# Optimization experiments

Hardware: AMD Instinct MI355X
Metric: run time of the kernel (lower is better)

The kernel has to match this reference:

```python
import jax, jax.numpy as jnp
import numpy as np

RRELU_SLOPE = (1.0 / 8.0 + 1.0 / 3.0) / 2.0  # RReLU eval-mode negative slope


def _layer(h, edge_feats, src, dst, W, b, Lw, Lb, n_nodes):
    # per-edge message: concat(src node feat, edge feat) -> linear
    msg = jnp.concatenate([h[src], edge_feats], axis=-1) @ W + b  # [E, H]
    # mean-aggregate messages by destination node (0 for isolated nodes, DGL semantics)
    s = jax.ops.segment_sum(msg, dst, num_segments=n_nodes)  # [N, H]
    cnt = jax.ops.segment_sum(jnp.ones((dst.shape[0], 1), msg.dtype), dst,
                              num_segments=n_nodes)  # [N, 1]
    agg = jnp.where(cnt > 0, s / jnp.maximum(cnt, 1.0), 0.0)
    # self-loop linear add
    agg = agg + h @ Lw + Lb
    # RReLU (eval mode = leaky relu with slope (lower+upper)/2); dropout p=0 is identity
    return jnp.where(agg >= 0, agg, agg * RRELU_SLOPE)


def setup_inputs() -> dict:
    key = jax.random.key(0)
    ks = jax.random.split(key, 12)
    N, E, D, H = 50000, 640000, 128, 128
    sc_in = 1.0 / np.sqrt(2 * D)
    sc_d = 1.0 / np.sqrt(D)
    sc_o = 1.0 / np.sqrt(2 * H)
    return {
        "node_feats": jax.random.normal(ks[0], (N, D), jnp.float32),
        "edge_feats": jax.random.normal(ks[1], (E, D), jnp.float32),
        "src": jax.random.randint(ks[2], (E,), 0, N),
        "dst": jax.random.randint(ks[3], (E,), 0, N),
        "W1": jax.random.uniform(ks[4], (2 * D, H), jnp.float32, -sc_in, sc_in),
        "b1": jnp.zeros((H,), jnp.float32),
        "L1": jax.random.uniform(ks[5], (D, H), jnp.float32, -sc_d, sc_d),
        "lb1": jnp.zeros((H,), jnp.float32),
        "W2": jax.random.uniform(ks[6], (2 * H, H), jnp.float32, -sc_in, sc_in),
        "b2": jnp.zeros((H,), jnp.float32),
        "L2": jax.random.uniform(ks[7], (H, H), jnp.float32, -sc_d, sc_d),
        "lb2": jnp.zeros((H,), jnp.float32),
        "Wo": jax.random.uniform(ks[8], (2 * H, H), jnp.float32, -sc_o, sc_o),
        "bo": jnp.zeros((H,), jnp.float32),
    }


def reference(node_feats, edge_feats, src, dst, W1, b1, L1, lb1, W2, b2, L2, lb2, Wo, bo):
    n = node_feats.shape[0]
    h1 = _layer(node_feats, edge_feats, src, dst, W1, b1, L1, lb1, n)
    h2 = _layer(h1, edge_feats, src, dst, W2, b2, L2, lb2, n)
    multihop = jnp.concatenate([h1, h2], axis=-1)  # [N, 2H]
    return multihop @ Wo + bo
```

## Files before the change

### kernel.cpp

```cpp
#include <hip/hip_runtime.h>
#include <hip/hip_bf16.h>

typedef unsigned short u16;
typedef unsigned int   u32;

using bf16x8 = __attribute__((ext_vector_type(8))) __bf16;
using f32x4  = __attribute__((ext_vector_type(4))) float;

#define SLOPE 0.22916666666666666f
#define CAP 64

static __device__ __forceinline__ u16 f2bf(float f) {
    u32 u = __float_as_uint(f);
    u += 0x7fffu + ((u >> 16) & 1u);
    return (u16)(u >> 16);
}
static __device__ __forceinline__ float bf2f(u16 h) {
    return __uint_as_float(((u32)h) << 16);
}

static __device__ __forceinline__ void gload_lds16(const u16* g, u16* l) {
    __builtin_amdgcn_global_load_lds(
        (const __attribute__((address_space(1))) void*)g,
        (__attribute__((address_space(3))) void*)l,
        16, 0, 0);
}

static __device__ __forceinline__ void add8(float* a, uint4 u) {
    a[0] += bf2f((u16)u.x); a[1] += bf2f((u16)(u.x >> 16));
    a[2] += bf2f((u16)u.y); a[3] += bf2f((u16)(u.y >> 16));
    a[4] += bf2f((u16)u.z); a[5] += bf2f((u16)(u.z >> 16));
    a[6] += bf2f((u16)u.w); a[7] += bf2f((u16)(u.w >> 16));
}

__global__ void k_prep(const int* __restrict__ src, const int* __restrict__ dst,
                       int* __restrict__ deg, int2* __restrict__ se,
                       const float* __restrict__ node, u16* __restrict__ nfb,
                       const float* __restrict__ W1, const float* __restrict__ L1,
                       const float* __restrict__ W2, const float* __restrict__ L2,
                       const float* __restrict__ Wo, u16* __restrict__ T,
                       int E, int n8, int gE, int gF) {
    int b = blockIdx.x, t = threadIdx.x;
    if (b < gE) {
        int i = b * 256 + t;
        if (i < E) {
            int d = dst[i];
            int p = atomicAdd(&deg[d], 1);
            if (p < CAP) se[(size_t)d * CAP + p] = make_int2(src[i], i);
        }
    } else if (b < gE + gF) {
        int i = (b - gE) * 256 + t;
        if (i < n8) {
            const float4* p = (const float4*)node + (size_t)i * 2;
            float4 a = p[0], c = p[1];
            union { u16 u[8]; uint4 v; } pk;
            pk.u[0] = f2bf(a.x); pk.u[1] = f2bf(a.y); pk.u[2] = f2bf(a.z); pk.u[3] = f2bf(a.w);
            pk.u[4] = f2bf(c.x); pk.u[5] = f2bf(c.y); pk.u[6] = f2bf(c.z); pk.u[7] = f2bf(c.w);
            *((uint4*)nfb + i) = pk.v;
        }
    } else {
        int m = b - gE - gF;
        const float* S; int rowoff;
        switch (m) {
            case 0: S = W1; rowoff = 0;   break;
            case 1: S = W1; rowoff = 128; break;
            case 2: S = L1; rowoff = 0;   break;
            case 3: S = W2; rowoff = 0;   break;
            case 4: S = W2; rowoff = 128; break;
            case 5: S = L2; rowoff = 0;   break;
            case 6: S = Wo; rowoff = 0;   break;
            default: S = Wo; rowoff = 128; break;
        }
        u16* O = T + m * 16384;
        for (int i = t; i < 16384; i += 256) {
            int c = i >> 7, k = i & 127;
            O[i] = f2bf(S[(rowoff + k) * 128 + c]);
        }
    }
}

__global__ void k_aggf(const float* __restrict__ ef, const u16* __restrict__ nfb,
                       const int2* __restrict__ se, const int* __restrict__ deg,
                       u16* __restrict__ EF, u16* __restrict__ A, int N) {
    int w = (blockIdx.x * blockDim.x + threadIdx.x) >> 6;
    int lane = threadIdx.x & 63;
    if (w >= N) return;
    int t4 = lane >> 4, qq = lane & 15;
    int d = deg[w];
    int dc = d < CAP ? d : CAP;
    const int2* sp = se + (size_t)w * CAP;
    float e[8] = {0.f, 0.f, 0.f, 0.f, 0.f, 0.f, 0.f, 0.f};
    float n[8] = {0.f, 0.f, 0.f, 0.f, 0.f, 0.f, 0.f, 0.f};
    int i = 0;
    for (; i + 8 <= dc; i += 8) {
        int2 iA = sp[i + t4], iB = sp[i + 4 + t4];
        const float* ra = ef + (size_t)iA.y * 128 + qq * 8;
        const float* rb = ef + (size_t)iB.y * 128 + qq * 8;
        float4 a0 = *(const float4*)ra, a1 = *(const float4*)(ra + 4);
        float4 c0 = *(const float4*)rb, c1 = *(const float4*)(rb + 4);
        uint4 ua = *(const uint4*)(nfb + (size_t)iA.x * 128 + qq * 8);
        uint4 ub = *(const uint4*)(nfb + (size_t)iB.x * 128 + qq * 8);
        e[0] += a0.x + c0.x; e[1] += a0.y + c0.y; e[2] += a0.z + c0.z; e[3] += a0.w + c0.w;
        e[4] += a1.x + c1.x; e[5] += a1.y + c1.y; e[6] += a1.z + c1.z; e[7] += a1.w + c1.w;
        add8(n, ua); add8(n, ub);
    }
    for (; i + 4 <= dc; i += 4) {
        int2 iA = sp[i + t4];
        const float* ra = ef + (size_t)iA.y * 128 + qq * 8;
        float4 a0 = *(const float4*)ra, a1 = *(const float4*)(ra + 4);
        uint4 ua = *(const uint4*)(nfb + (size_t)iA.x * 128 + qq * 8);
        e[0] += a0.x; e[1] += a0.y; e[2] += a0.z; e[3] += a0.w;
        e[4] += a1.x; e[5] += a1.y; e[6] += a1.z; e[7] += a1.w;
        add8(n, ua);
    }
    if (i + t4 < dc) {
        int2 iA = sp[i + t4];
        const float* ra = ef + (size_t)iA.y * 128 + qq * 8;
        float4 a0 = *(const float4*)ra, a1 = *(const float4*)(ra + 4);
        uint4 ua = *(const uint4*)(nfb + (size_t)iA.x * 128 + qq * 8);
        e[0] += a0.x; e[1] += a0.y; e[2] += a0.z; e[3] += a0.w;
        e[4] += a1.x; e[5] += a1.y; e[6] += a1.z; e[7] += a1.w;
        add8(n, ua);
    }
    #pragma unroll
    for (int j = 0; j < 8; j++) {
        e[j] += __shfl_xor(e[j], 16); e[j] += __shfl_xor(e[j], 32);
        n[j] += __shfl_xor(n[j], 16); n[j] += __shfl_xor(n[j], 32);
    }
    float sc = d > 0 ? 1.0f / (float)d : 0.0f;
    if (t4 == 0) {
        union { u16 u[8]; uint4 v; } pk;
        #pragma unroll
        for (int j = 0; j < 8; j++) pk.u[j] = f2bf(e[j] * sc);
        *(uint4*)(EF + (size_t)w * 128 + qq * 8) = pk.v;
    } else if (t4 == 1) {
        union { u16 u[8]; uint4 v; } pk;
        #pragma unroll
        for (int j = 0; j < 8; j++) pk.u[j] = f2bf(n[j] * sc);
        *(uint4*)(A + (size_t)w * 128 + qq * 8) = pk.v;
    }
}

__global__ void k_aggb(const u16* __restrict__ h, const int2* __restrict__ se,
                       const int* __restrict__ deg, u16* __restrict__ out, int N) {
    int w = (blockIdx.x * blockDim.x + threadIdx.x) >> 6;
    int lane = threadIdx.x & 63;
    if (w >= N) return;
    int quarter = lane >> 4, q = lane & 15;
    int d = deg[w];
    int dc = d < CAP ? d : CAP;
    const int2* sp = se + (size_t)w * CAP;
    float a[8] = {0.f, 0.f, 0.f, 0.f, 0.f, 0.f, 0.f, 0.f};
    int i = 0;
    for (; i + 8 <= dc; i += 8) {
        int eA = sp[i + quarter].x, eB = sp[i + 4 + quarter].x;
        uint4 uA = *(const uint4*)(h + (size_t)eA * 128 + q * 8);
        uint4 uB = *(const uint4*)(h + (size_t)eB * 128 + q * 8);
        add8(a, uA); add8(a, uB);
    }
    for (; i + 4 <= dc; i += 4) {
        int eA = sp[i + quarter].x;
        uint4 uA = *(const uint4*)(h + (size_t)eA * 128 + q * 8);
        add8(a, uA);
    }
    if (i + quarter < dc) {
        int eA = sp[i + quarter].x;
        uint4 uA = *(const uint4*)(h + (size_t)eA * 128 + q * 8);
        add8(a, uA);
    }
    #pragma unroll
    for (int j = 0; j < 8; j++) {
        a[j] += __shfl_xor(a[j], 32);
        a[j] += __shfl_xor(a[j], 16);
    }
    if (quarter == 0) {
        float sc = d > 0 ? 1.0f / (float)d : 0.0f;
        union { u16 u[8]; uint4 v; } pk;
        #pragma unroll
        for (int j = 0; j < 8; j++) pk.u[j] = f2bf(a[j] * sc);
        *(uint4*)(out + (size_t)w * 128 + q * 8) = pk.v;
    }
}

#define STAGE_X128(LBUF, GPTR)                                                      \
    {                                                                               \
        _Pragma("unroll")                                                           \
        for (int i_ = 0; i_ < 4; i_++) {                                            \
            int id_ = t + i_ * 512;                                                 \
            int r_ = id_ >> 4, c16_ = id_ & 15;                                     \
            int rg_ = row0 + r_; if (rg_ >= N) rg_ = N - 1;                         \
            gload_lds16((GPTR) + (size_t)rg_ * 128 + ((c16_ ^ (r_ & 15)) << 3),     \
                        (LBUF) + id_ * 8);                                          \
        }                                                                           \
    }
#define STAGE_W512(GPTR)                                                            \
    {                                                                               \
        _Pragma("unroll")                                                           \
        for (int i_ = 0; i_ < 4; i_++) {                                            \
            int id_ = t + i_ * 512;                                                 \
            int cc_ = id_ >> 4, c16_ = id_ & 15;                                    \
            gload_lds16((GPTR) + cc_ * 128 + ((c16_ ^ (cc_ & 15)) << 3),            \
                        Wl + id_ * 8);                                              \
        }                                                                           \
    }
#define COMPUTE(LBUF)                                                               \
    {                                                                               \
        _Pragma("unroll")                                                           \
        for (int ks_ = 0; ks_ < 4; ks_++) {                                         \
            bf16x8 af_[2], bf_[4];                                                  \
            _Pragma("unroll")                                                       \
            for (int h_ = 0; h_ < 2; h_++) {                                        \
                int r_ = wr * 32 + h_ * 16 + lanelo;                                \
                int ch_ = (ks_ * 4 + lanehi) ^ (r_ & 15);                           \
                af_[h_] = *(const bf16x8*)((LBUF) + r_ * 128 + ch_ * 8);            \
            }                                                                       \
            _Pragma("unroll")                                                       \
            for (int g_ = 0; g_ < 4; g_++) {                                        \
                int cc_ = wc * 64 + g_ * 16 + lanelo;                               \
                int ch_ = (ks_ * 4 + lanehi) ^ (cc_ & 15);                          \
                bf_[g_] = *(const bf16x8*)(Wl + cc_ * 128 + ch_ * 8);               \
            }                                                                       \
            _Pragma("unroll")                                                       \
            for (int h_ = 0; h_ < 2; h_++)                                          \
                _Pragma("unroll")                                                   \
                for (int g_ = 0; g_ < 4; g_++)                                      \
                    acc[h_][g_] = __builtin_amdgcn_mfma_f32_16x16x32_bf16(          \
                        af_[h_], bf_[g_], acc[h_][g_], 0, 0, 0);                    \
        }                                                                           \
    }

__global__ __launch_bounds__(512, 4) void k_gemm3s(
    const u16* __restrict__ X0, const u16* __restrict__ X1, const u16* __restrict__ X2,
    const u16* __restrict__ T0, const u16* __restrict__ T1, const u16* __restrict__ T2,
    const float* __restrict__ bm, const int* __restrict__ deg,
    const float* __restrict__ ba, u16* __restrict__ outp, int N) {

    __shared__ u16 XB[128 * 128];
    __shared__ u16 Wl[128 * 128];

    int t = threadIdx.x, lane = t & 63, wid = t >> 6;
    int lanelo = lane & 15, lanehi = lane >> 4;
    int wr = wid >> 1, wc = wid & 1;
    int row0 = blockIdx.x * 128;

    f32x4 acc[2][4];
    #pragma unroll
    for (int h = 0; h < 2; h++)
        #pragma unroll
        for (int g = 0; g < 4; g++) acc[h][g] = (f32x4){0.f, 0.f, 0.f, 0.f};

    STAGE_X128(XB, X0);
    STAGE_W512(T0);
    __syncthreads();
    COMPUTE(XB);
    __syncthreads();
    STAGE_X128(XB, X1);
    STAGE_W512(T1);
    __syncthreads();
    COMPUTE(XB);
    __syncthreads();
    STAGE_X128(XB, X2);
    STAGE_W512(T2);
    __syncthreads();
    COMPUTE(XB);

    #pragma unroll
    for (int h = 0; h < 2; h++) {
        #pragma unroll
        for (int r = 0; r < 4; r++) {
            int rowt = wr * 32 + h * 16 + lanehi * 4 + r;
            int rg = row0 + rowt;
            if (rg >= N) continue;
            float m = (deg[rg] > 0) ? 1.f : 0.f;
            #pragma unroll
            for (int g = 0; g < 4; g++) {
                int col = wc * 64 + g * 16 + lanelo;
                float v = acc[h][g][r] + ba[col] + m * bm[col];
                v = (v >= 0.f) ? v : v * SLOPE;
                outp[(size_t)rg * 128 + col] = f2bf(v);
            }
        }
    }
}

__global__ __launch_bounds__(512, 4) void k_gemmo(
    const u16* __restrict__ X0, const u16* __restrict__ X1,
    const u16* __restrict__ T0, const u16* __restrict__ T1,
    const float* __restrict__ ba, float* __restrict__ outp, int N) {

    __shared__ u16 XB[128 * 128];
    __shared__ u16 Wl[128 * 128];

    int t = threadIdx.x, lane = t & 63, wid = t >> 6;
    int lanelo = lane & 15, lanehi = lane >> 4;
    int wr = wid >> 1, wc = wid & 1;
    int row0 = blockIdx.x * 128;

    f32x4 acc[2][4];
    #pragma unroll
    for (int h = 0; h < 2; h++)
        #pragma unroll
        for (int g = 0; g < 4; g++) acc[h][g] = (f32x4){0.f, 0.f, 0.f, 0.f};

    STAGE_X128(XB, X0);
    STAGE_W512(T0);
    __syncthreads();
    COMPUTE(XB);
    __syncthreads();
    STAGE_X128(XB, X1);
    STAGE_W512(T1);
    __syncthreads();
    COMPUTE(XB);

    #pragma unroll
    for (int h = 0; h < 2; h++) {
        #pragma unroll
        for (int r = 0; r < 4; r++) {
            int rowt = wr * 32 + h * 16 + lanehi * 4 + r;
            int rg = row0 + rowt;
            if (rg >= N) continue;
            #pragma unroll
            for (int g = 0; g < 4; g++) {
                int col = wc * 64 + g * 16 + lanelo;
                outp[(size_t)rg * 128 + col] = acc[h][g][r] + ba[col];
            }
        }
    }
}


extern "C" void kernel_launch(void* const* d_in, const int* in_sizes, int n_in,
                              void* d_out, int out_size, void* d_ws, size_t ws_size,
                              hipStream_t stream) {
    const float* node = (const float*)d_in[0];
    const float* ef   = (const float*)d_in[1];
    const int*   src  = (const int*)d_in[2];
    const int*   dst  = (const int*)d_in[3];
    const float* W1   = (const float*)d_in[4];
    const float* b1   = (const float*)d_in[5];
    const float* L1   = (const float*)d_in[6];
    const float* lb1  = (const float*)d_in[7];
    const float* W2   = (const float*)d_in[8];
    const float* b2   = (const float*)d_in[9];
    const float* L2   = (const float*)d_in[10];
    const float* lb2  = (const float*)d_in[11];
    const float* Wo   = (const float*)d_in[12];
    const float* bo   = (const float*)d_in[13];
    int N = in_sizes[0] / 128;
    int E = in_sizes[2];

    char* ws = (char*)d_ws;
    size_t o = 0;
    auto alloc = [&](size_t bytes) {
        void* p = ws + o;
        o = (o + bytes + 511) & ~(size_t)511;
        return p;
    };
    int*  deg = (int*)alloc((size_t)N * 4);
    int2* se  = (int2*)alloc((size_t)N * CAP * 8);
    u16*  T   = (u16*)alloc((size_t)8 * 16384 * 2);
    u16*  nfb = (u16*)alloc((size_t)N * 128 * 2);
    u16*  EF  = (u16*)alloc((size_t)N * 128 * 2);
    u16*  A   = (u16*)alloc((size_t)N * 128 * 2);
    u16*  h1  = (u16*)alloc((size_t)N * 128 * 2);
    u16*  h2  = (u16*)alloc((size_t)N * 128 * 2);

    hipMemsetAsync(deg, 0, (size_t)N * 4, stream);

    int gE = (E + 255) / 256;
    int n8 = N * 128 / 8;
    int gF = (n8 + 255) / 256;
    k_prep<<<gE + gF + 8, 256, 0, stream>>>(src, dst, deg, se, node, nfb,
                                            W1, L1, W2, L2, Wo, T, E, n8, gE, gF);

    int gA = (N + 3) / 4;
    k_aggf<<<gA, 256, 0, stream>>>(ef, nfb, se, deg, EF, A, N);

    int gb = (N + 127) / 128;
    k_gemm3s<<<gb, 512, 0, stream>>>(A, EF, nfb, T, T + 16384, T + 2 * 16384,
                                     b1, deg, lb1, h1, N);
    k_aggb<<<gA, 256, 0, stream>>>(h1, se, deg, A, N);
    k_gemm3s<<<gb, 512, 0, stream>>>(A, EF, h1, T + 3 * 16384, T + 4 * 16384, T + 5 * 16384,
                                     b2, deg, lb2, h2, N);
    k_gemmo<<<gb, 512, 0, stream>>>(h1, h2, T + 6 * 16384, T + 7 * 16384,
                                    bo, (float*)d_out, N);
}
```

Measured before the change: 203.4 us.

## Store only edge ids in CSR buckets and look up src indirectly

The per-destination bucket array now holds only the edge index instead of an (src, edge) pair, which halves its size and the scatter writes in the prep kernel. The aggregation kernels fetch the source node through an extra dependent load from the src array. The prep fill has each thread handle two edges to overlap atomics, and the weight transpose is split across 64 blocks instead of 8. The trade-off is an extra indirect gather latency in both aggregation kernels, set against less write traffic during prep.

```diff
diff --git a/kernel.cpp b/kernel.cpp
--- a/kernel.cpp
+++ b/kernel.cpp
@@ -33,23 +33,26 @@
     a[6] += bf2f((u16)u.w); a[7] += bf2f((u16)(u.w >> 16));
 }
 
-__global__ void k_prep(const int* __restrict__ src, const int* __restrict__ dst,
-                       int* __restrict__ deg, int2* __restrict__ se,
-                       const float* __restrict__ node, u16* __restrict__ nfb,
+__global__ void k_prep(const int* __restrict__ dst, int* __restrict__ deg,
+                       int* __restrict__ se, const float* __restrict__ node,
+                       u16* __restrict__ nfb,
                        const float* __restrict__ W1, const float* __restrict__ L1,
                        const float* __restrict__ W2, const float* __restrict__ L2,
                        const float* __restrict__ Wo, u16* __restrict__ T,
-                       int E, int n8, int gE, int gF) {
+                       int E, int halfE, int n8, int gFill, int gF) {
     int b = blockIdx.x, t = threadIdx.x;
-    if (b < gE) {
-        int i = b * 256 + t;
-        if (i < E) {
-            int d = dst[i];
-            int p = atomicAdd(&deg[d], 1);
-            if (p < CAP) se[(size_t)d * CAP + p] = make_int2(src[i], i);
-        }
-    } else if (b < gE + gF) {
-        int i = (b - gE) * 256 + t;
+    if (b < gFill) {
+        int i0 = b * 256 + t;
+        int i1 = i0 + halfE;
+        int d0 = -1, d1 = -1;
+        if (i0 < halfE) d0 = dst[i0];
+        if (i1 < E)     d1 = dst[i1];
+        int p0 = (d0 >= 0) ? atomicAdd(&deg[d0], 1) : 0;
+        int p1 = (d1 >= 0) ? atomicAdd(&deg[d1], 1) : 0;
+        if (d0 >= 0 && p0 < CAP) se[(size_t)d0 * CAP + p0] = i0;
+        if (d1 >= 0 && p1 < CAP) se[(size_t)d1 * CAP + p1] = i1;
+    } else if (b < gFill + gF) {
+        int i = (b - gFill) * 256 + t;
         if (i < n8) {
             const float4* p = (const float4*)node + (size_t)i * 2;
             float4 a = p[0], c = p[1];
@@ -59,7 +62,8 @@
             *((uint4*)nfb + i) = pk.v;
         }
     } else {
-        int m = b - gE - gF;
+        int mb = b - gFill - gF;
+        int m = mb >> 3, chunk = mb & 7;
         const float* S; int rowoff;
         switch (m) {
             case 0: S = W1; rowoff = 0;   break;
@@ -72,15 +76,17 @@
             default: S = Wo; rowoff = 128; break;
         }
         u16* O = T + m * 16384;
-        for (int i = t; i < 16384; i += 256) {
-            int c = i >> 7, k = i & 127;
-            O[i] = f2bf(S[(rowoff + k) * 128 + c]);
+        int j0 = chunk * 2048, j1 = j0 + 2048;
+        for (int j = j0 + t; j < j1; j += 256) {
+            int c = j >> 7, k = j & 127;
+            O[j] = f2bf(S[(rowoff + k) * 128 + c]);
         }
     }
 }
 
 __global__ void k_aggf(const float* __restrict__ ef, const u16* __restrict__ nfb,
-                       const int2* __restrict__ se, const int* __restrict__ deg,
+                       const int* __restrict__ se, const int* __restrict__ srcA,
+                       const int* __restrict__ deg,
                        u16* __restrict__ EF, u16* __restrict__ A, int N) {
     int w = (blockIdx.x * blockDim.x + threadIdx.x) >> 6;
     int lane = threadIdx.x & 63;
@@ -88,36 +94,39 @@
     int t4 = lane >> 4, qq = lane & 15;
     int d = deg[w];
     int dc = d < CAP ? d : CAP;
-    const int2* sp = se + (size_t)w * CAP;
+    const int* sp = se + (size_t)w * CAP;
     float e[8] = {0.f, 0.f, 0.f, 0.f, 0.f, 0.f, 0.f, 0.f};
     float n[8] = {0.f, 0.f, 0.f, 0.f, 0.f, 0.f, 0.f, 0.f};
     int i = 0;
     for (; i + 8 <= dc; i += 8) {
-        int2 iA = sp[i + t4], iB = sp[i + 4 + t4];
-        const float* ra = ef + (size_t)iA.y * 128 + qq * 8;
-        const float* rb = ef + (size_t)iB.y * 128 + qq * 8;
+        int eA = sp[i + t4], eB = sp[i + 4 + t4];
+        int sA = srcA[eA], sB = srcA[eB];
+        const float* ra = ef + (size_t)eA * 128 + qq * 8;
+        const float* rb = ef + (size_t)eB * 128 + qq * 8;
         float4 a0 = *(const float4*)ra, a1 = *(const float4*)(ra + 4);
         float4 c0 = *(const float4*)rb, c1 = *(const float4*)(rb + 4);
-        uint4 ua = *(const uint4*)(nfb + (size_t)iA.x * 128 + qq * 8);
-        uint4 ub = *(const uint4*)(nfb + (size_t)iB.x * 128 + qq * 8);
+        uint4 ua = *(const uint4*)(nfb + (size_t)sA * 128 + qq * 8);
+        uint4 ub = *(const uint4*)(nfb + (size_t)sB * 128 + qq * 8);
         e[0] += a0.x + c0.x; e[1] += a0.y + c0.y; e[2] += a0.z + c0.z; e[3] += a0.w + c0.w;
         e[4] += a1.x + c1.x; e[5] += a1.y + c1.y; e[6] += a1.z + c1.z; e[7] += a1.w + c1.w;
         add8(n, ua); add8(n, ub);
     }
     for (; i + 4 <= dc; i += 4) {
-        int2 iA = sp[i + t4];
-        const float* ra = ef + (size_t)iA.y * 128 + qq * 8;
+        int eA = sp[i + t4];
+        int sA = srcA[eA];
+        const float* ra = ef + (size_t)eA * 128 + qq * 8;
         float4 a0 = *(const float4*)ra, a1 = *(const float4*)(ra + 4);
-        uint4 ua = *(const uint4*)(nfb + (size_t)iA.x * 128 + qq * 8);
+        uint4 ua = *(const uint4*)(nfb + (size_t)sA * 128 + qq * 8);
         e[0] += a0.x; e[1] += a0.y; e[2] += a0.z; e[3] += a0.w;
         e[4] += a1.x; e[5] += a1.y; e[6] += a1.z; e[7] += a1.w;
         add8(n, ua);
     }
     if (i + t4 < dc) {
-        int2 iA = sp[i + t4];
-        const float* ra = ef + (size_t)iA.y * 128 + qq * 8;
+        int eA = sp[i + t4];
+        int sA = srcA[eA];
+        const float* ra = ef + (size_t)eA * 128 + qq * 8;
         float4 a0 = *(const float4*)ra, a1 = *(const float4*)(ra + 4);
-        uint4 ua = *(const uint4*)(nfb + (size_t)iA.x * 128 + qq * 8);
+        uint4 ua = *(const uint4*)(nfb + (size_t)sA * 128 + qq * 8);
         e[0] += a0.x; e[1] += a0.y; e[2] += a0.z; e[3] += a0.w;
         e[4] += a1.x; e[5] += a1.y; e[6] += a1.z; e[7] += a1.w;
         add8(n, ua);
@@ -141,31 +150,32 @@
     }
 }
 
-__global__ void k_aggb(const u16* __restrict__ h, const int2* __restrict__ se,
-                       const int* __restrict__ deg, u16* __restrict__ out, int N) {
+__global__ void k_aggb(const u16* __restrict__ h, const int* __restrict__ se,
+                       const int* __restrict__ srcA, const int* __restrict__ deg,
+                       u16* __restrict__ out, int N) {
     int w = (blockIdx.x * blockDim.x + threadIdx.x) >> 6;
     int lane = threadIdx.x & 63;
     if (w >= N) return;
     int quarter = lane >> 4, q = lane & 15;
     int d = deg[w];
     int dc = d < CAP ? d : CAP;
-    const int2* sp = se + (size_t)w * CAP;
+    const int* sp = se + (size_t)w * CAP;
     float a[8] = {0.f, 0.f, 0.f, 0.f, 0.f, 0.f, 0.f, 0.f};
     int i = 0;
     for (; i + 8 <= dc; i += 8) {
-        int eA = sp[i + quarter].x, eB = sp[i + 4 + quarter].x;
-        uint4 uA = *(const uint4*)(h + (size_t)eA * 128 + q * 8);
-        uint4 uB = *(const uint4*)(h + (size_t)eB * 128 + q * 8);
+        int sA = srcA[sp[i + quarter]], sB = srcA[sp[i + 4 + quarter]];
+        uint4 uA = *(const uint4*)(h + (size_t)sA * 128 + q * 8);
+        uint4 uB = *(const uint4*)(h + (size_t)sB * 128 + q * 8);
         add8(a, uA); add8(a, uB);
     }
     for (; i + 4 <= dc; i += 4) {
-        int eA = sp[i + quarter].x;
-        uint4 uA = *(const uint4*)(h + (size_t)eA * 128 + q * 8);
+        int sA = srcA[sp[i + quarter]];
+        uint4 uA = *(const uint4*)(h + (size_t)sA * 128 + q * 8);
         add8(a, uA);
     }
     if (i + quarter < dc) {
-        int eA = sp[i + quarter].x;
-        uint4 uA = *(const uint4*)(h + (size_t)eA * 128 + q * 8);
+        int sA = srcA[sp[i + quarter]];
+        uint4 uA = *(const uint4*)(h + (size_t)sA * 128 + q * 8);
         add8(a, uA);
     }
     #pragma unroll
@@ -357,7 +367,7 @@
         return p;
     };
     int*  deg = (int*)alloc((size_t)N * 4);
-    int2* se  = (int2*)alloc((size_t)N * CAP * 8);
+    int*  se  = (int*)alloc((size_t)N * CAP * 4);
     u16*  T   = (u16*)alloc((size_t)8 * 16384 * 2);
     u16*  nfb = (u16*)alloc((size_t)N * 128 * 2);
     u16*  EF  = (u16*)alloc((size_t)N * 128 * 2);
@@ -367,19 +377,21 @@
 
     hipMemsetAsync(deg, 0, (size_t)N * 4, stream);
 
-    int gE = (E + 255) / 256;
+    int halfE = (E + 1) / 2;
+    int gFill = (halfE + 255) / 256;
     int n8 = N * 128 / 8;
     int gF = (n8 + 255) / 256;
-    k_prep<<<gE + gF + 8, 256, 0, stream>>>(src, dst, deg, se, node, nfb,
-                                            W1, L1, W2, L2, Wo, T, E, n8, gE, gF);
+    k_prep<<<gFill + gF + 64, 256, 0, stream>>>(dst, deg, se, node, nfb,
+                                                W1, L1, W2, L2, Wo, T,
+                                                E, halfE, n8, gFill, gF);
 
     int gA = (N + 3) / 4;
-    k_aggf<<<gA, 256, 0, stream>>>(ef, nfb, se, deg, EF, A, N);
+    k_aggf<<<gA, 256, 0, stream>>>(ef, nfb, se, src, deg, EF, A, N);
 
     int gb = (N + 127) / 128;
     k_gemm3s<<<gb, 512, 0, stream>>>(A, EF, nfb, T, T + 16384, T + 2 * 16384,
                                      b1, deg, lb1, h1, N);
-    k_aggb<<<gA, 256, 0, stream>>>(h1, se, deg, A, N);
+    k_aggb<<<gA, 256, 0, stream>>>(h1, se, src, deg, A, N);
     k_gemm3s<<<gb, 512, 0, stream>>>(A, EF, h1, T + 3 * 16384, T + 4 * 16384, T + 5 * 16384,
                                      b2, deg, lb2, h2, N);
     k_gemmo<<<gb, 512, 0, stream>>>(h1, h2, T + 6 * 16384, T + 7 * 16384,
```

Result: slower. 208.9 us (+2.7%).

## Replace capped per-node edge buckets with exact CSR built by count-scan-fill

Applied to the files above, without the earlier changes.

Swaps the fixed-capacity per-destination edge slots (CAP=64) for a compact CSR. Degrees are counted, prefix-scanned across three small kernels into offsets, and a second atomic pass fills edges into place. This drops the 64-entry cap, so every edge is now aggregated, and makes the adjacency lists contiguous. In exchange it adds four kernel launches and a second atomic pass over the edges, and weight transposition is now split over more blocks.

```diff
diff --git a/kernel.cpp b/kernel.cpp
--- a/kernel.cpp
+++ b/kernel.cpp
@@ -8,7 +8,6 @@
 using f32x4  = __attribute__((ext_vector_type(4))) float;
 
 #define SLOPE 0.22916666666666666f
-#define CAP 64
 
 static __device__ __forceinline__ u16 f2bf(float f) {
     u32 u = __float_as_uint(f);
@@ -33,8 +32,7 @@
     a[6] += bf2f((u16)u.w); a[7] += bf2f((u16)(u.w >> 16));
 }
 
-__global__ void k_prep(const int* __restrict__ src, const int* __restrict__ dst,
-                       int* __restrict__ deg, int2* __restrict__ se,
+__global__ void k_prep(const int* __restrict__ dst, int* __restrict__ deg,
                        const float* __restrict__ node, u16* __restrict__ nfb,
                        const float* __restrict__ W1, const float* __restrict__ L1,
                        const float* __restrict__ W2, const float* __restrict__ L2,
@@ -43,11 +41,7 @@
     int b = blockIdx.x, t = threadIdx.x;
     if (b < gE) {
         int i = b * 256 + t;
-        if (i < E) {
-            int d = dst[i];
-            int p = atomicAdd(&deg[d], 1);
-            if (p < CAP) se[(size_t)d * CAP + p] = make_int2(src[i], i);
-        }
+        if (i < E) atomicAdd(&deg[dst[i]], 1);
     } else if (b < gE + gF) {
         int i = (b - gE) * 256 + t;
         if (i < n8) {
@@ -59,7 +53,8 @@
             *((uint4*)nfb + i) = pk.v;
         }
     } else {
-        int m = b - gE - gF;
+        int mb = b - gE - gF;
+        int m = mb >> 3, chunk = mb & 7;
         const float* S; int rowoff;
         switch (m) {
             case 0: S = W1; rowoff = 0;   break;
@@ -72,27 +67,113 @@
             default: S = Wo; rowoff = 128; break;
         }
         u16* O = T + m * 16384;
-        for (int i = t; i < 16384; i += 256) {
-            int c = i >> 7, k = i & 127;
-            O[i] = f2bf(S[(rowoff + k) * 128 + c]);
-        }
+        int j0 = chunk * 2048, j1 = j0 + 2048;
+        for (int j = j0 + t; j < j1; j += 256) {
+            int c = j >> 7, k = j & 127;
+            O[j] = f2bf(S[(rowoff + k) * 128 + c]);
+        }
+    }
+}
+
+__global__ void k_scan1(const int* __restrict__ deg, int* __restrict__ bsum, int N) {
+    __shared__ int ws[4];
+    int b = blockIdx.x, t = threadIdx.x, lane = t & 63, w = t >> 6;
+    int base = b * 1024 + t * 4;
+    int4 v = {0, 0, 0, 0};
+    if (base + 4 <= N) v = *(const int4*)(deg + base);
+    else if (base < N) {
+        v.x = deg[base];
+        if (base + 1 < N) v.y = deg[base + 1];
+        if (base + 2 < N) v.z = deg[base + 2];
+    }
+    int tsum = v.x + v.y + v.z + v.w;
+    #pragma unroll
+    for (int d = 1; d < 64; d <<= 1) tsum += __shfl_xor(tsum, d);
+    if (lane == 0) ws[w] = tsum;
+    __syncthreads();
+    if (t == 0) bsum[b] = ws[0] + ws[1] + ws[2] + ws[3];
+}
+
+__global__ void k_scan2(const int* __restrict__ bsum, int* __restrict__ bbase,
+                        int* __restrict__ off, int NB, int N) {
+    int lane = threadIdx.x;
+    int base = 0;
+    for (int c = 0; c < NB; c += 64) {
+        int i = c + lane;
+        int v = (i < NB) ? bsum[i] : 0;
+        int incl = v;
+        #pragma unroll
+        for (int d = 1; d < 64; d <<= 1) {
+            int y = __shfl_up(incl, d);
+            if (lane >= d) incl += y;
+        }
+        if (i < NB) bbase[i] = base + incl - v;
+        base += __shfl(incl, 63);
+    }
+    if (lane == 0) off[N] = base;
+}
+
+__global__ void k_scan3(const int* __restrict__ deg, const int* __restrict__ bbase,
+                        int* __restrict__ off, int* __restrict__ cursor, int N) {
+    __shared__ int ws[4];
+    int b = blockIdx.x, t = threadIdx.x, lane = t & 63, w = t >> 6;
+    int base = b * 1024 + t * 4;
+    int4 v = {0, 0, 0, 0};
+    if (base + 4 <= N) v = *(const int4*)(deg + base);
+    else if (base < N) {
+        v.x = deg[base];
+        if (base + 1 < N) v.y = deg[base + 1];
+        if (base + 2 < N) v.z = deg[base + 2];
+    }
+    int tsum = v.x + v.y + v.z + v.w;
+    int incl = tsum;
+    #pragma unroll
+    for (int d = 1; d < 64; d <<= 1) {
+        int y = __shfl_up(incl, d);
+        if (lane >= d) incl += y;
+    }
+    if (lane == 63) ws[w] = incl;
+    __syncthreads();
+    int wbase = 0;
+    #pragma unroll
+    for (int i = 0; i < 4; i++) if (i < w) wbase += ws[i];
+    int e = bbase[b] + wbase + incl - tsum;
+    int4 o;
+    o.x = e; o.y = e + v.x; o.z = o.y + v.y; o.w = o.z + v.z;
+    if (base + 4 <= N) {
+        *(int4*)(off + base) = o;
+        *(int4*)(cursor + base) = o;
+    } else if (base < N) {
+        off[base] = o.x; cursor[base] = o.x;
+        if (base + 1 < N) { off[base + 1] = o.y; cursor[base + 1] = o.y; }
+        if (base + 2 < N) { off[base + 2] = o.z; cursor[base + 2] = o.z; }
+    }
+}
+
+__global__ void k_fill(const int* __restrict__ src, const int* __restrict__ dst,
+                       int* __restrict__ cursor, int2* __restrict__ csr, int E) {
+    int i = blockIdx.x * 256 + threadIdx.x;
+    if (i < E) {
+        int d = dst[i];
+        int p = atomicAdd(&cursor[d], 1);
+        csr[p] = make_int2(src[i], i);
     }
 }
 
 __global__ void k_aggf(const float* __restrict__ ef, const u16* __restrict__ nfb,
-                       const int2* __restrict__ se, const int* __restrict__ deg,
+                       const int2* __restrict__ csr, const int* __restrict__ off,
+                       const int* __restrict__ deg,
                        u16* __restrict__ EF, u16* __restrict__ A, int N) {
     int w = (blockIdx.x * blockDim.x + threadIdx.x) >> 6;
     int lane = threadIdx.x & 63;
     if (w >= N) return;
     int t4 = lane >> 4, qq = lane & 15;
     int d = deg[w];
-    int dc = d < CAP ? d : CAP;
-    const int2* sp = se + (size_t)w * CAP;
+    const int2* sp = csr + off[w];
     float e[8] = {0.f, 0.f, 0.f, 0.f, 0.f, 0.f, 0.f, 0.f};
     float n[8] = {0.f, 0.f, 0.f, 0.f, 0.f, 0.f, 0.f, 0.f};
     int i = 0;
-    for (; i + 8 <= dc; i += 8) {
+    for (; i + 8 <= d; i += 8) {
         int2 iA = sp[i + t4], iB = sp[i + 4 + t4];
         const float* ra = ef + (size_t)iA.y * 128 + qq * 8;
         const float* rb = ef + (size_t)iB.y * 128 + qq * 8;
@@ -104,7 +185,7 @@
         e[4] += a1.x + c1.x; e[5] += a1.y + c1.y; e[6] += a1.z + c1.z; e[7] += a1.w + c1.w;
         add8(n, ua); add8(n, ub);
     }
-    for (; i + 4 <= dc; i += 4) {
+    for (; i + 4 <= d; i += 4) {
         int2 iA = sp[i + t4];
         const float* ra = ef + (size_t)iA.y * 128 + qq * 8;
         float4 a0 = *(const float4*)ra, a1 = *(const float4*)(ra + 4);
@@ -113,7 +194,7 @@
         e[4] += a1.x; e[5] += a1.y; e[6] += a1.z; e[7] += a1.w;
         add8(n, ua);
     }
-    if (i + t4 < dc) {
+    if (i + t4 < d) {
         int2 iA = sp[i + t4];
         const float* ra = ef + (size_t)iA.y * 128 + qq * 8;
         float4 a0 = *(const float4*)ra, a1 = *(const float4*)(ra + 4);
@@ -141,29 +222,29 @@
     }
 }
 
-__global__ void k_aggb(const u16* __restrict__ h, const int2* __restrict__ se,
-                       const int* __restrict__ deg, u16* __restrict__ out, int N) {
+__global__ void k_aggb(const u16* __restrict__ h, const int2* __restrict__ csr,
+                       const int* __restrict__ off, const int* __restrict__ deg,
+                       u16* __restrict__ out, int N) {
     int w = (blockIdx.x * blockDim.x + threadIdx.x) >> 6;
     int lane = threadIdx.x & 63;
     if (w >= N) return;
     int quarter = lane >> 4, q = lane & 15;
     int d = deg[w];
-    int dc = d < CAP ? d : CAP;
-    const int2* sp = se + (size_t)w * CAP;
+    const int2* sp = csr + off[w];
     float a[8] = {0.f, 0.f, 0.f, 0.f, 0.f, 0.f, 0.f, 0.f};
     int i = 0;
-    for (; i + 8 <= dc; i += 8) {
+    for (; i + 8 <= d; i += 8) {
         int eA = sp[i + quarter].x, eB = sp[i + 4 + quarter].x;
         uint4 uA = *(const uint4*)(h + (size_t)eA * 128 + q * 8);
         uint4 uB = *(const uint4*)(h + (size_t)eB * 128 + q * 8);
         add8(a, uA); add8(a, uB);
     }
-    for (; i + 4 <= dc; i += 4) {
+    for (; i + 4 <= d; i += 4) {
         int eA = sp[i + quarter].x;
         uint4 uA = *(const uint4*)(h + (size_t)eA * 128 + q * 8);
         add8(a, uA);
     }
-    if (i + quarter < dc) {
+    if (i + quarter < d) {
         int eA = sp[i + quarter].x;
         uint4 uA = *(const uint4*)(h + (size_t)eA * 128 + q * 8);
         add8(a, uA);
@@ -348,6 +429,7 @@
     const float* bo   = (const float*)d_in[13];
     int N = in_sizes[0] / 128;
     int E = in_sizes[2];
+    int NB = (N + 1023) / 1024;
 
     char* ws = (char*)d_ws;
     size_t o = 0;
@@ -356,30 +438,38 @@
         o = (o + bytes + 511) & ~(size_t)511;
         return p;
     };
-    int*  deg = (int*)alloc((size_t)N * 4);
-    int2* se  = (int2*)alloc((size_t)N * CAP * 8);
-    u16*  T   = (u16*)alloc((size_t)8 * 16384 * 2);
-    u16*  nfb = (u16*)alloc((size_t)N * 128 * 2);
-    u16*  EF  = (u16*)alloc((size_t)N * 128 * 2);
-    u16*  A   = (u16*)alloc((size_t)N * 128 * 2);
-    u16*  h1  = (u16*)alloc((size_t)N * 128 * 2);
-    u16*  h2  = (u16*)alloc((size_t)N * 128 * 2);
+    int*  deg    = (int*)alloc((size_t)N * 4);
+    int*  off    = (int*)alloc((size_t)(N + 1) * 4);
+    int*  cursor = (int*)alloc((size_t)N * 4);
+    int*  bsum   = (int*)alloc((size_t)NB * 4);
+    int*  bbase  = (int*)alloc((size_t)NB * 4);
+    int2* csr    = (int2*)alloc((size_t)E * 8);
+    u16*  T      = (u16*)alloc((size_t)8 * 16384 * 2);
+    u16*  nfb    = (u16*)alloc((size_t)N * 128 * 2);
+    u16*  EF     = (u16*)alloc((size_t)N * 128 * 2);
+    u16*  A      = (u16*)alloc((size_t)N * 128 * 2);
+    u16*  h1     = (u16*)alloc((size_t)N * 128 * 2);
+    u16*  h2     = (u16*)alloc((size_t)N * 128 * 2);
 
     hipMemsetAsync(deg, 0, (size_t)N * 4, stream);
 
     int gE = (E + 255) / 256;
     int n8 = N * 128 / 8;
     int gF = (n8 + 255) / 256;
-    k_prep<<<gE + gF + 8, 256, 0, stream>>>(src, dst, deg, se, node, nfb,
-                                            W1, L1, W2, L2, Wo, T, E, n8, gE, gF);
+    k_prep<<<gE + gF + 64, 256, 0, stream>>>(dst, deg, node, nfb,
+                                             W1, L1, W2, L2, Wo, T, E, n8, gE, gF);
+    k_scan1<<<NB, 256, 0, stream>>>(deg, bsum, N);
+    k_scan2<<<1, 64, 0, stream>>>(bsum, bbase, off, NB, N);
+    k_scan3<<<NB, 256, 0, stream>>>(deg, bbase, off, cursor, N);
+    k_fill<<<gE, 256, 0, stream>>>(src, dst, cursor, csr, E);
 
     int gA = (N + 3) / 4;
-    k_aggf<<<gA, 256, 0, stream>>>(ef, nfb, se, deg, EF, A, N);
+    k_aggf<<<gA, 256, 0, stream>>>(ef, nfb, csr, off, deg, EF, A, N);
 
     int gb = (N + 127) / 128;
     k_gemm3s<<<gb, 512, 0, stream>>>(A, EF, nfb, T, T + 16384, T + 2 * 16384,
                                      b1, deg, lb1, h1, N);
-    k_aggb<<<gA, 256, 0, stream>>>(h1, se, deg, A, N);
+    k_aggb<<<gA, 256, 0, stream>>>(h1, csr, off, deg, A, N);
     k_gemm3s<<<gb, 512, 0, stream>>>(A, EF, h1, T + 3 * 16384, T + 4 * 16384, T + 5 * 16384,
                                      b2, deg, lb2, h2, N);
     k_gemmo<<<gb, 512, 0, stream>>>(h1, h2, T + 6 * 16384, T + 7 * 16384,
```

After: 236.0 us. 16.0% more time.

## Build per-node edge lists via atomicExch linked lists and split weight transpose

Applied to the files above, without the earlier changes.

Replaces the atomicAdd-slot scatter into the padded per-node edge table with a lock-free linked list built by atomicExch on a head array, followed by a new per-node kernel that walks each list to fill the padded table and degree array. The weight-transpose work in the prep kernel is also split across 64 blocks instead of 8 so it no longer leaves a few long-running blocks at the tail. This adds an extra kernel launch and pointer-chasing dependent loads in the list walk, and the edge order within each node's list now follows atomic completion order, which could change accumulation order and therefore rounding.

```diff
diff --git a/kernel.cpp b/kernel.cpp
--- a/kernel.cpp
+++ b/kernel.cpp
@@ -34,7 +34,7 @@
 }
 
 __global__ void k_prep(const int* __restrict__ src, const int* __restrict__ dst,
-                       int* __restrict__ deg, int2* __restrict__ se,
+                       int* __restrict__ head, int2* __restrict__ link,
                        const float* __restrict__ node, u16* __restrict__ nfb,
                        const float* __restrict__ W1, const float* __restrict__ L1,
                        const float* __restrict__ W2, const float* __restrict__ L2,
@@ -45,8 +45,8 @@
         int i = b * 256 + t;
         if (i < E) {
             int d = dst[i];
-            int p = atomicAdd(&deg[d], 1);
-            if (p < CAP) se[(size_t)d * CAP + p] = make_int2(src[i], i);
+            int prev = atomicExch(&head[d], i);
+            link[i] = make_int2(prev, src[i]);
         }
     } else if (b < gE + gF) {
         int i = (b - gE) * 256 + t;
@@ -59,7 +59,8 @@
             *((uint4*)nfb + i) = pk.v;
         }
     } else {
-        int m = b - gE - gF;
+        int mb = b - gE - gF;
+        int m = mb >> 3, chunk = mb & 7;
         const float* S; int rowoff;
         switch (m) {
             case 0: S = W1; rowoff = 0;   break;
@@ -72,11 +73,28 @@
             default: S = Wo; rowoff = 128; break;
         }
         u16* O = T + m * 16384;
-        for (int i = t; i < 16384; i += 256) {
-            int c = i >> 7, k = i & 127;
-            O[i] = f2bf(S[(rowoff + k) * 128 + c]);
-        }
-    }
+        int j0 = chunk * 2048, j1 = j0 + 2048;
+        for (int j = j0 + t; j < j1; j += 256) {
+            int c = j >> 7, k = j & 127;
+            O[j] = f2bf(S[(rowoff + k) * 128 + c]);
+        }
+    }
+}
+
+__global__ void k_mklist(const int* __restrict__ head, const int2* __restrict__ link,
+                         int2* __restrict__ se, int* __restrict__ deg, int N) {
+    int w = blockIdx.x * 256 + threadIdx.x;
+    if (w >= N) return;
+    int2* bp = se + (size_t)w * CAP;
+    int e = head[w];
+    int cnt = 0;
+    while (e >= 0) {
+        int2 pr = link[e];
+        if (cnt < CAP) bp[cnt] = make_int2(pr.y, e);
+        e = pr.x;
+        cnt++;
+    }
+    deg[w] = cnt;
 }
 
 __global__ void k_aggf(const float* __restrict__ ef, const u16* __restrict__ nfb,
@@ -356,22 +374,25 @@
         o = (o + bytes + 511) & ~(size_t)511;
         return p;
     };
-    int*  deg = (int*)alloc((size_t)N * 4);
-    int2* se  = (int2*)alloc((size_t)N * CAP * 8);
-    u16*  T   = (u16*)alloc((size_t)8 * 16384 * 2);
-    u16*  nfb = (u16*)alloc((size_t)N * 128 * 2);
-    u16*  EF  = (u16*)alloc((size_t)N * 128 * 2);
-    u16*  A   = (u16*)alloc((size_t)N * 128 * 2);
-    u16*  h1  = (u16*)alloc((size_t)N * 128 * 2);
-    u16*  h2  = (u16*)alloc((size_t)N * 128 * 2);
-
-    hipMemsetAsync(deg, 0, (size_t)N * 4, stream);
+    int*  head = (int*)alloc((size_t)N * 4);
+    int2* link = (int2*)alloc((size_t)E * 8);
+    int2* se   = (int2*)alloc((size_t)N * CAP * 8);
+    int*  deg  = (int*)alloc((size_t)N * 4);
+    u16*  T    = (u16*)alloc((size_t)8 * 16384 * 2);
+    u16*  nfb  = (u16*)alloc((size_t)N * 128 * 2);
+    u16*  EF   = (u16*)alloc((size_t)N * 128 * 2);
+    u16*  A    = (u16*)alloc((size_t)N * 128 * 2);
+    u16*  h1   = (u16*)alloc((size_t)N * 128 * 2);
+    u16*  h2   = (u16*)alloc((size_t)N * 128 * 2);
+
+    hipMemsetAsync(head, 0xFF, (size_t)N * 4, stream);
 
     int gE = (E + 255) / 256;
     int n8 = N * 128 / 8;
     int gF = (n8 + 255) / 256;
-    k_prep<<<gE + gF + 8, 256, 0, stream>>>(src, dst, deg, se, node, nfb,
-                                            W1, L1, W2, L2, Wo, T, E, n8, gE, gF);
+    k_prep<<<gE + gF + 64, 256, 0, stream>>>(src, dst, head, link, node, nfb,
+                                             W1, L1, W2, L2, Wo, T, E, n8, gE, gF);
+    k_mklist<<<(N + 255) / 256, 256, 0, stream>>>(head, link, se, deg, N);
 
     int gA = (N + 3) / 4;
     k_aggf<<<gA, 256, 0, stream>>>(ef, nfb, se, deg, EF, A, N);
```

Measured after the change: 207.5 us. 1.02x slower.
